# Optimization experiments

Hardware: AMD Instinct MI355X
Metric: run time of the kernel (lower is better)

Reference implementation:

```python
import jax, jax.numpy as jnp
import numpy as np
import math

A, B, C, D = 32, 32, 8, 16
K, STRIDE, PAD, ITERS = 3, 1, 1, 3
KK = K * K
KKA = KK * A


def squash(s, axis=-1):
    mag_sq = jnp.sum(s ** 2, axis=axis, keepdims=True)
    mag = jnp.sqrt(mag_sq)
    return mag_sq / (1.0 + mag_sq) * (s / mag)


def setup_inputs() -> dict:
    key = jax.random.key(0)
    k1, k2 = jax.random.split(key)
    pose = jax.random.normal(k1, (4, A * C, 14, 14), dtype=jnp.float32)
    # kaiming_uniform_ on (KKA, B*D, C): fan_in = (B*D)*C = 4096, bound = sqrt(6/fan_in)
    bound = math.sqrt(6.0 / (B * D * C))
    W = jax.random.uniform(k2, (KKA, B * D, C), dtype=jnp.float32, minval=-bound, maxval=bound)
    return {"pose": pose, "W": W}


def reference(pose, W):
    b, _, h, w = pose.shape
    # F.unfold equivalent: (b, A*C*kk, oh, ow), channel-major then kernel-position ordering
    patches = jax.lax.conv_general_dilated_patches(
        pose, (K, K), (STRIDE, STRIDE), [(PAD, PAD), (PAD, PAD)])
    l = patches.shape[2] * patches.shape[3]
    x = patches.reshape(b, A, C, KK, l)
    x = jnp.transpose(x, (0, 4, 3, 1, 2)).reshape(b, l, KKA, C)  # (b,l,kkA,C)
    # pose_out[b,l,k,:] = W[k] @ x[b,l,k]  -> (b,l,kkA,B*D)
    pose_out = jnp.einsum('kpc,blkc->blkp', W, x).reshape(b, l, KKA, B, D)
    logits = jnp.zeros((b, l, KKA, B, 1), dtype=pose.dtype)
    v = None
    for _ in range(ITERS):
        c = jax.nn.softmax(logits, axis=3)                      # over B capsules
        s = jnp.sum(c * pose_out, axis=2, keepdims=True)        # (b,l,1,B,D)
        v = squash(s)
        logits = logits + jnp.sum(v * pose_out, axis=-1, keepdims=True)
    v = v[:, :, 0]                                              # (b,l,B,D)
    v = jnp.transpose(v.reshape(b, l, B * D), (0, 2, 1))        # (b,B*D,l)
    oh = math.isqrt(l)
    return v.reshape(b, B * D, oh, oh)
```

## Files before the change

### kernel.cpp

```cpp
#include <hip/hip_runtime.h>
#include <stdint.h>

#define NSITES 784
#define LSZ    196
#define HWD    14
#define KKA_   288
#define BD_    512
#define NRG    6
#define ROWS_PER_BLK 48
#define NW     8
#define ROWS_PER_WAVE 6
#define SITES_PER_BLK 4
#define KC     6

#define WH_OFF    0
#define XH_OFF    2359296
#define WG_OFF    5971968
#define S1_OFF    8331264
#define PART_OFF  9936896
#define VBUF_OFF  19570688
#define WS_NEED   21176320

typedef _Float16 h2 __attribute__((ext_vector_type(2)));
typedef _Float16 h8 __attribute__((ext_vector_type(8)));
typedef float    f4 __attribute__((ext_vector_type(4)));

#define PIN8(p) asm volatile("" : "+v"(p[0]),"+v"(p[1]),"+v"(p[2]),"+v"(p[3]), \
                                  "+v"(p[4]),"+v"(p[5]),"+v"(p[6]),"+v"(p[7]))

__device__ __forceinline__ float dot8(const uint4 wv, const uint4 xv) {
    h2 w0 = __builtin_bit_cast(h2, wv.x), w1 = __builtin_bit_cast(h2, wv.y),
       w2 = __builtin_bit_cast(h2, wv.z), w3 = __builtin_bit_cast(h2, wv.w);
    h2 x0 = __builtin_bit_cast(h2, xv.x), x1 = __builtin_bit_cast(h2, xv.y),
       x2 = __builtin_bit_cast(h2, xv.z), x3 = __builtin_bit_cast(h2, xv.w);
#if __has_builtin(__builtin_amdgcn_fdot2)
    float acc = __builtin_amdgcn_fdot2(w0, x0, 0.f, false);
    acc = __builtin_amdgcn_fdot2(w1, x1, acc, false);
    acc = __builtin_amdgcn_fdot2(w2, x2, acc, false);
    acc = __builtin_amdgcn_fdot2(w3, x3, acc, false);
    return acc;
#else
    float acc = (float)w0.x*(float)x0.x + (float)w0.y*(float)x0.y
              + (float)w1.x*(float)x1.x + (float)w1.y*(float)x1.y
              + (float)w2.x*(float)x2.x + (float)w2.y*(float)x2.y
              + (float)w3.x*(float)x3.x + (float)w3.y*(float)x3.y;
    return acc;
#endif
}

__global__ __launch_bounds__(256) void k_prep(
    const float* __restrict__ pose, const float* __restrict__ W,
    uint4* __restrict__ Wh, uint4* __restrict__ xh, uint4* __restrict__ Wg)
{
    const int t  = threadIdx.x;
    const int bx = blockIdx.x;
    if (bx < NSITES) {
        const int site = bx;
        const int b = site / LSZ;
        const int l = site - b * LSZ;
        const int oh = l / HWD, ow = l - oh * HWD;
        for (int kk = t; kk < KKA_; kk += 256) {
            const int p = kk >> 5, a = kk & 31;
            const int ky = p / 3 - 1, kx = p % 3 - 1;
            const int y = oh + ky, x = ow + kx;
            const bool inb = (y >= 0 && y < HWD && x >= 0 && x < HWD);
            const float* pp = pose + ((size_t)b * 256 + a * 8) * LSZ
                            + (inb ? (y * HWD + x) : 0);
            uint32_t uo[4];
            #pragma unroll
            for (int cp = 0; cp < 4; ++cp) {
                const float f0 = inb ? pp[(2*cp)   * LSZ] : 0.f;
                const float f1 = inb ? pp[(2*cp+1) * LSZ] : 0.f;
                h2 hh; hh.x = (_Float16)f0; hh.y = (_Float16)f1;
                uo[cp] = __builtin_bit_cast(uint32_t, hh);
            }
            uint4 o; o.x = uo[0]; o.y = uo[1]; o.z = uo[2]; o.w = uo[3];
            xh[(size_t)site * KKA_ + kk] = o;
        }
    } else {
        const int wb = bx - NSITES;
        const int kk = wb * 4 + (t >> 6);
        const int ln = t & 63;
        const float* Wr = W + (size_t)kk * (BD_ * 8);
        #pragma unroll
        for (int u = 0; u < 8; ++u) {
            const int p = ln * 8 + u;
            const float4 fa = *(const float4*)(Wr + p * 8);
            const float4 fb = *(const float4*)(Wr + p * 8 + 4);
            uint32_t uo[4];
            h2 h0; h0.x=(_Float16)fa.x; h0.y=(_Float16)fa.y; uo[0]=__builtin_bit_cast(uint32_t,h0);
            h2 h1; h1.x=(_Float16)fa.z; h1.y=(_Float16)fa.w; uo[1]=__builtin_bit_cast(uint32_t,h1);
            h2 hv; hv.x=(_Float16)fb.x; hv.y=(_Float16)fb.y; uo[2]=__builtin_bit_cast(uint32_t,hv);
            h2 h3; h3.x=(_Float16)fb.z; h3.y=(_Float16)fb.w; uo[3]=__builtin_bit_cast(uint32_t,h3);
            uint4 o; o.x=uo[0]; o.y=uo[1]; o.z=uo[2]; o.w=uo[3];
            Wh[(size_t)kk * 512 + u * 64 + ln] = o;
            Wg[(size_t)kk * 512 + p] = o;
        }
    }
}

__global__ __launch_bounds__(256) void k_gemm1(
    const uint4* __restrict__ xh, const uint4* __restrict__ Wg,
    float* __restrict__ s1p)
{
    const int t   = threadIdx.x;
    const int w   = t >> 6;
    const int l   = t & 63;
    const int m0  = blockIdx.x * 16;
    const int n0  = blockIdx.y * 64 + w * 16;
    const int kc  = blockIdx.z;
    const int row = l & 15;
    const int sub = l >> 4;

    f4 acc = {0.f, 0.f, 0.f, 0.f};
    const uint4* ap = xh + (size_t)(m0 + row) * KKA_ + kc * 48 + sub;
    const uint4* bp = Wg + ((size_t)kc * 48 + sub) * 512 + (n0 + row);

    #pragma unroll
    for (int ks = 0; ks < 12; ++ks) {
        const h8 a = __builtin_bit_cast(h8, ap[ks * 4]);
        const h8 b = __builtin_bit_cast(h8, bp[(size_t)ks * 4 * 512]);
        acc = __builtin_amdgcn_mfma_f32_16x16x32_f16(a, b, acc, 0, 0, 0);
    }

    float* op = s1p + (size_t)kc * (NSITES * BD_)
              + (size_t)(m0 + sub * 4) * BD_ + n0 + row;
    op[0]        = acc[0];
    op[BD_]      = acc[1];
    op[2 * BD_]  = acc[2];
    op[3 * BD_]  = acc[3];
}

__global__ __launch_bounds__(256) void k_red1(
    const float* __restrict__ s1p, float* __restrict__ vbuf)
{
    const int site = blockIdx.x * 4 + (threadIdx.x >> 6);
    const int ln = threadIdx.x & 63;
    float tv[8] = {0.f,0.f,0.f,0.f,0.f,0.f,0.f,0.f};
    #pragma unroll
    for (int kc = 0; kc < KC; ++kc) {
        const float4* sp = (const float4*)(s1p + (size_t)kc * (NSITES * BD_)
                                           + (size_t)site * BD_ + ln * 8);
        const float4 a = sp[0], b = sp[1];
        tv[0]+=a.x; tv[1]+=a.y; tv[2]+=a.z; tv[3]+=a.w;
        tv[4]+=b.x; tv[5]+=b.y; tv[6]+=b.z; tv[7]+=b.w;
    }
    float msq = 0.f;
    #pragma unroll
    for (int j = 0; j < 8; ++j) { tv[j] *= (1.f / 32.f); msq += tv[j] * tv[j]; }
    msq += __shfl_xor(msq, 1, 64);
    const float fac = sqrtf(msq) / (1.f + msq);
    #pragma unroll
    for (int j = 0; j < 8; ++j) vbuf[(size_t)site * BD_ + ln * 8 + j] = tv[j] * fac;
}

template<int PASS>
__global__ __launch_bounds__(512, 4) void k_sweep(
    const uint4* __restrict__ Wh, const uint4* __restrict__ xh,
    const float* __restrict__ vbuf, float* __restrict__ partial)
{
    const int t  = threadIdx.x;
    const int w  = t >> 6;
    const int ln = t & 63;
    const int sg = blockIdx.x;
    const int rg = blockIdx.y;
    const int site0 = sg * SITES_PER_BLK;
    const int kk0 = __builtin_amdgcn_readfirstlane(rg * ROWS_PER_BLK + w);

    float v[SITES_PER_BLK][8];
    #pragma unroll
    for (int s = 0; s < SITES_PER_BLK; ++s) {
        const float4* vp = (const float4*)(vbuf + (size_t)(site0 + s) * BD_ + ln * 8);
        const float4 a = vp[0], bq = vp[1];
        v[s][0]=a.x;  v[s][1]=a.y;  v[s][2]=a.z;  v[s][3]=a.w;
        v[s][4]=bq.x; v[s][5]=bq.y; v[s][6]=bq.z; v[s][7]=bq.w;
        PIN8(v[s]);
    }

    float sacc[SITES_PER_BLK][8];
    #pragma unroll
    for (int s = 0; s < SITES_PER_BLK; ++s)
        #pragma unroll
        for (int j = 0; j < 8; ++j) sacc[s][j] = 0.f;

    const uint4* Wrow = Wh + (size_t)kk0 * 512;
    const uint4* xrow = xh + kk0;

    #pragma unroll 1
    for (int r = 0; r < ROWS_PER_WAVE; ++r) {
        uint4 wr[8];
        #pragma unroll
        for (int u = 0; u < 8; ++u) wr[u] = Wrow[u * 64 + ln];
        Wrow += NW * 512;

        #pragma unroll
        for (int s = 0; s < SITES_PER_BLK; ++s) {
            const uint4 xr = xrow[(size_t)(site0 + s) * KKA_];
            float po[8];
            #pragma unroll
            for (int j = 0; j < 8; ++j) po[j] = dot8(wr[j], xr);
            float up = v[s][0] * po[0];
            #pragma unroll
            for (int j = 1; j < 8; ++j) up += v[s][j] * po[j];
            up += __shfl_xor(up, 1, 64);
            const float e = __expf(up);
            float se = e;
            se += __shfl_xor(se, 2, 64);
            se += __shfl_xor(se, 4, 64);
            se += __shfl_xor(se, 8, 64);
            se += __shfl_xor(se, 16, 64);
            se += __shfl_xor(se, 32, 64);
            const float c = e * __builtin_amdgcn_rcpf(se);
            #pragma unroll
            for (int j = 0; j < 8; ++j) sacc[s][j] += c * po[j];
        }
        xrow += NW;
    }

    __shared__ float red[NW * BD_];
    #pragma unroll
    for (int s = 0; s < SITES_PER_BLK; ++s) {
        if (s) __syncthreads();
        float4 r0, r1;
        r0.x=sacc[s][0]; r0.y=sacc[s][1]; r0.z=sacc[s][2]; r0.w=sacc[s][3];
        r1.x=sacc[s][4]; r1.y=sacc[s][5]; r1.z=sacc[s][6]; r1.w=sacc[s][7];
        *(float4*)&red[w * BD_ + ln * 8]     = r0;
        *(float4*)&red[w * BD_ + ln * 8 + 4] = r1;
        __syncthreads();
        {
            const int p = t;
            float acc = red[p];
            #pragma unroll
            for (int ww = 1; ww < NW; ++ww) acc += red[ww * BD_ + p];
            partial[((size_t)(site0 + s) * NRG + rg) * BD_ + p] = acc;
        }
    }
}

template<int PASS>
__global__ __launch_bounds__(256) void k_reduce(
    const float* __restrict__ partial, float* __restrict__ vbuf,
    float* __restrict__ out)
{
    const int site = blockIdx.x * 4 + (threadIdx.x >> 6);
    const int ln = threadIdx.x & 63;
    float tv[8] = {0.f,0.f,0.f,0.f,0.f,0.f,0.f,0.f};
    #pragma unroll
    for (int rg = 0; rg < NRG; ++rg) {
        const float4* pp4 = (const float4*)(partial + ((size_t)site * NRG + rg) * BD_ + ln * 8);
        const float4 a = pp4[0], b = pp4[1];
        tv[0]+=a.x; tv[1]+=a.y; tv[2]+=a.z; tv[3]+=a.w;
        tv[4]+=b.x; tv[5]+=b.y; tv[6]+=b.z; tv[7]+=b.w;
    }
    float msq = 0.f;
    #pragma unroll
    for (int j = 0; j < 8; ++j) msq += tv[j] * tv[j];
    msq += __shfl_xor(msq, 1, 64);
    const float fac = sqrtf(msq) / (1.f + msq);
    if (PASS == 2) {
        #pragma unroll
        for (int j = 0; j < 8; ++j) vbuf[(size_t)site * BD_ + ln * 8 + j] += tv[j] * fac;
    } else {
        const int b = site / LSZ;
        const int l = site - b * LSZ;
        float* op = out + (size_t)b * BD_ * LSZ + l;
        #pragma unroll
        for (int j = 0; j < 8; ++j) op[(size_t)(ln * 8 + j) * LSZ] = tv[j] * fac;
    }
}

extern "C" void kernel_launch(void* const* d_in, const int* in_sizes, int n_in,
                              void* d_out, int out_size, void* d_ws, size_t ws_size,
                              hipStream_t stream) {
    const float* pose = (const float*)d_in[0];
    const float* W    = (const float*)d_in[1];
    float* out        = (float*)d_out;

    if (ws_size < (size_t)WS_NEED) return;

    uint8_t* ws = (uint8_t*)d_ws;
    uint4*  Wh     = (uint4*)  (ws + WH_OFF);
    uint4*  xh     = (uint4*)  (ws + XH_OFF);
    uint4*  Wg     = (uint4*)  (ws + WG_OFF);
    float* partial = (float*)  (ws + PART_OFF);
    float* vbuf    = (float*)  (ws + VBUF_OFF);

    k_prep<<<dim3(NSITES + 72), dim3(256), 0, stream>>>(pose, W, Wh, xh, Wg);

    k_gemm1<<<dim3(49, 8, KC), dim3(256), 0, stream>>>(xh, Wg, partial);
    k_red1<<<dim3(NSITES / 4), dim3(256), 0, stream>>>(partial, vbuf);

    const dim3 gs(NSITES / SITES_PER_BLK, NRG);
    k_sweep<2><<<gs, dim3(512), 0, stream>>>(Wh, xh, vbuf, partial);
    k_reduce<2><<<dim3(NSITES / 4), dim3(256), 0, stream>>>(partial, vbuf, out);
    k_sweep<3><<<gs, dim3(512), 0, stream>>>(Wh, xh, vbuf, partial);
    k_reduce<3><<<dim3(NSITES / 4), dim3(256), 0, stream>>>(partial, vbuf, out);
}
```

Baseline: 179.3 us.

## Repartition sweep into 8 row groups of 6 waves and linearize grids

The sweep kernel now uses 8 row groups of 36 rows with 6 waves (384 threads) per block instead of 6 groups of 48 rows with 8 waves, and the first GEMM splits K into 8 chunks instead of 6. Both grids are flattened to 1D, with the K-chunk or row-group index in the low bits so neighbouring blocks share the same sites/tiles for better L2 locality. The GEMM output moves to its own workspace buffer so it no longer aliases the partial buffer. This adds more blocks and more partials for the reduce kernels to sum, and the 512-wide cross-wave reduction now loops over 384 threads.

```diff
diff --git a/kernel.cpp b/kernel.cpp
--- a/kernel.cpp
+++ b/kernel.cpp
@@ -6,20 +6,20 @@
 #define HWD    14
 #define KKA_   288
 #define BD_    512
-#define NRG    6
-#define ROWS_PER_BLK 48
-#define NW     8
+#define NRG    8
+#define ROWS_PER_BLK 36
+#define NW     6
 #define ROWS_PER_WAVE 6
 #define SITES_PER_BLK 4
-#define KC     6
+#define KC     8
 
 #define WH_OFF    0
 #define XH_OFF    2359296
 #define WG_OFF    5971968
-#define S1_OFF    8331264
-#define PART_OFF  9936896
-#define VBUF_OFF  19570688
-#define WS_NEED   21176320
+#define GP_OFF    8331264
+#define PART_OFF  21176320
+#define VBUF_OFF  34021376
+#define WS_NEED   35627008
 
 typedef _Float16 h2 __attribute__((ext_vector_type(2)));
 typedef _Float16 h8 __attribute__((ext_vector_type(8)));
@@ -101,29 +101,33 @@
 
 __global__ __launch_bounds__(256) void k_gemm1(
     const uint4* __restrict__ xh, const uint4* __restrict__ Wg,
-    float* __restrict__ s1p)
-{
+    float* __restrict__ gp)
+{
+    const int bid = blockIdx.x;
+    const int kc  = bid & 7;
+    const int r2  = bid >> 3;
+    const int nb  = r2 & 7;
+    const int mb  = r2 >> 3;
     const int t   = threadIdx.x;
     const int w   = t >> 6;
     const int l   = t & 63;
-    const int m0  = blockIdx.x * 16;
-    const int n0  = blockIdx.y * 64 + w * 16;
-    const int kc  = blockIdx.z;
+    const int m0  = mb * 16;
+    const int n0  = nb * 64 + w * 16;
     const int row = l & 15;
     const int sub = l >> 4;
 
     f4 acc = {0.f, 0.f, 0.f, 0.f};
-    const uint4* ap = xh + (size_t)(m0 + row) * KKA_ + kc * 48 + sub;
-    const uint4* bp = Wg + ((size_t)kc * 48 + sub) * 512 + (n0 + row);
-
-    #pragma unroll
-    for (int ks = 0; ks < 12; ++ks) {
+    const uint4* ap = xh + (size_t)(m0 + row) * KKA_ + kc * 36 + sub;
+    const uint4* bp = Wg + ((size_t)kc * 36 + sub) * 512 + (n0 + row);
+
+    #pragma unroll
+    for (int ks = 0; ks < 9; ++ks) {
         const h8 a = __builtin_bit_cast(h8, ap[ks * 4]);
         const h8 b = __builtin_bit_cast(h8, bp[(size_t)ks * 4 * 512]);
         acc = __builtin_amdgcn_mfma_f32_16x16x32_f16(a, b, acc, 0, 0, 0);
     }
 
-    float* op = s1p + (size_t)kc * (NSITES * BD_)
+    float* op = gp + (size_t)kc * (NSITES * BD_)
               + (size_t)(m0 + sub * 4) * BD_ + n0 + row;
     op[0]        = acc[0];
     op[BD_]      = acc[1];
@@ -132,14 +136,14 @@
 }
 
 __global__ __launch_bounds__(256) void k_red1(
-    const float* __restrict__ s1p, float* __restrict__ vbuf)
+    const float* __restrict__ gp, float* __restrict__ vbuf)
 {
     const int site = blockIdx.x * 4 + (threadIdx.x >> 6);
     const int ln = threadIdx.x & 63;
     float tv[8] = {0.f,0.f,0.f,0.f,0.f,0.f,0.f,0.f};
     #pragma unroll
     for (int kc = 0; kc < KC; ++kc) {
-        const float4* sp = (const float4*)(s1p + (size_t)kc * (NSITES * BD_)
+        const float4* sp = (const float4*)(gp + (size_t)kc * (NSITES * BD_)
                                            + (size_t)site * BD_ + ln * 8);
         const float4 a = sp[0], b = sp[1];
         tv[0]+=a.x; tv[1]+=a.y; tv[2]+=a.z; tv[3]+=a.w;
@@ -155,15 +159,16 @@
 }
 
 template<int PASS>
-__global__ __launch_bounds__(512, 4) void k_sweep(
+__global__ __launch_bounds__(384, 4) void k_sweep(
     const uint4* __restrict__ Wh, const uint4* __restrict__ xh,
     const float* __restrict__ vbuf, float* __restrict__ partial)
 {
+    const int bid = blockIdx.x;
+    const int rg  = bid & 7;
+    const int sg  = bid >> 3;
     const int t  = threadIdx.x;
     const int w  = t >> 6;
     const int ln = t & 63;
-    const int sg = blockIdx.x;
-    const int rg = blockIdx.y;
     const int site0 = sg * SITES_PER_BLK;
     const int kk0 = __builtin_amdgcn_readfirstlane(rg * ROWS_PER_BLK + w);
 
@@ -227,8 +232,7 @@
         *(float4*)&red[w * BD_ + ln * 8]     = r0;
         *(float4*)&red[w * BD_ + ln * 8 + 4] = r1;
         __syncthreads();
-        {
-            const int p = t;
+        for (int p = t; p < BD_; p += 384) {
             float acc = red[p];
             #pragma unroll
             for (int ww = 1; ww < NW; ++ww) acc += red[ww * BD_ + p];
@@ -282,17 +286,18 @@
     uint4*  Wh     = (uint4*)  (ws + WH_OFF);
     uint4*  xh     = (uint4*)  (ws + XH_OFF);
     uint4*  Wg     = (uint4*)  (ws + WG_OFF);
+    float*  gp     = (float*)  (ws + GP_OFF);
     float* partial = (float*)  (ws + PART_OFF);
     float* vbuf    = (float*)  (ws + VBUF_OFF);
 
     k_prep<<<dim3(NSITES + 72), dim3(256), 0, stream>>>(pose, W, Wh, xh, Wg);
 
-    k_gemm1<<<dim3(49, 8, KC), dim3(256), 0, stream>>>(xh, Wg, partial);
-    k_red1<<<dim3(NSITES / 4), dim3(256), 0, stream>>>(partial, vbuf);
-
-    const dim3 gs(NSITES / SITES_PER_BLK, NRG);
-    k_sweep<2><<<gs, dim3(512), 0, stream>>>(Wh, xh, vbuf, partial);
+    k_gemm1<<<dim3(49 * 8 * KC), dim3(256), 0, stream>>>(xh, Wg, gp);
+    k_red1<<<dim3(NSITES / 4), dim3(256), 0, stream>>>(gp, vbuf);
+
+    const dim3 gs(196 * NRG);
+    k_sweep<2><<<gs, dim3(384), 0, stream>>>(Wh, xh, vbuf, partial);
     k_reduce<2><<<dim3(NSITES / 4), dim3(256), 0, stream>>>(partial, vbuf, out);
-    k_sweep<3><<<gs, dim3(512), 0, stream>>>(Wh, xh, vbuf, partial);
+    k_sweep<3><<<gs, dim3(384), 0, stream>>>(Wh, xh, vbuf, partial);
     k_reduce<3><<<dim3(NSITES / 4), dim3(256), 0, stream>>>(partial, vbuf, out);
 }
```

New measurement: 203.9 us. 13.7% more time.

## Coalesce pose unfold reads in prep and stage x tiles in LDS for gemm1

Applied to the files above, without the earlier changes.

The prep kernel's unfold is remapped so each block handles one (batch, kernel-position, capsule) triple and its threads walk the 196 spatial sites. Consecutive threads now read adjacent pose addresses instead of strided ones, but the xh writes become strided. The gemm1 kernel first loads its 16x48 x tile into padded LDS, so the four waves share one global load instead of each fetching it. This costs a block barrier and some LDS. An unused offset define is dropped and a parameter renamed.

```diff
diff --git a/kernel.cpp b/kernel.cpp
--- a/kernel.cpp
+++ b/kernel.cpp
@@ -16,7 +16,6 @@
 #define WH_OFF    0
 #define XH_OFF    2359296
 #define WG_OFF    5971968
-#define S1_OFF    8331264
 #define PART_OFF  9936896
 #define VBUF_OFF  19570688
 #define WS_NEED   21176320
@@ -54,14 +53,14 @@
 {
     const int t  = threadIdx.x;
     const int bx = blockIdx.x;
-    if (bx < NSITES) {
-        const int site = bx;
-        const int b = site / LSZ;
-        const int l = site - b * LSZ;
-        const int oh = l / HWD, ow = l - oh * HWD;
-        for (int kk = t; kk < KKA_; kk += 256) {
-            const int p = kk >> 5, a = kk & 31;
-            const int ky = p / 3 - 1, kx = p % 3 - 1;
+    if (bx < 4 * KKA_) {
+        const int b  = bx / KKA_;
+        const int kk = bx - b * KKA_;
+        const int p  = kk >> 5, a = kk & 31;
+        const int ky = p / 3 - 1, kx = p % 3 - 1;
+        if (t < LSZ) {
+            const int l  = t;
+            const int oh = l / HWD, ow = l - oh * HWD;
             const int y = oh + ky, x = ow + kx;
             const bool inb = (y >= 0 && y < HWD && x >= 0 && x < HWD);
             const float* pp = pose + ((size_t)b * 256 + a * 8) * LSZ
@@ -75,10 +74,10 @@
                 uo[cp] = __builtin_bit_cast(uint32_t, hh);
             }
             uint4 o; o.x = uo[0]; o.y = uo[1]; o.z = uo[2]; o.w = uo[3];
-            xh[(size_t)site * KKA_ + kk] = o;
+            xh[((size_t)b * LSZ + l) * KKA_ + kk] = o;
         }
     } else {
-        const int wb = bx - NSITES;
+        const int wb = bx - 4 * KKA_;
         const int kk = wb * 4 + (t >> 6);
         const int ln = t & 63;
         const float* Wr = W + (size_t)kk * (BD_ * 8);
@@ -101,7 +100,7 @@
 
 __global__ __launch_bounds__(256) void k_gemm1(
     const uint4* __restrict__ xh, const uint4* __restrict__ Wg,
-    float* __restrict__ s1p)
+    float* __restrict__ gp)
 {
     const int t   = threadIdx.x;
     const int w   = t >> 6;
@@ -112,18 +111,26 @@
     const int row = l & 15;
     const int sub = l >> 4;
 
+    __shared__ uint4 x_lds[16][49];
+    #pragma unroll
+    for (int q = 0; q < 3; ++q) {
+        const int idx = t + 256 * q;
+        const int r = idx / 48, i = idx - r * 48;
+        x_lds[r][i] = xh[(size_t)(m0 + r) * KKA_ + kc * 48 + i];
+    }
+    __syncthreads();
+
     f4 acc = {0.f, 0.f, 0.f, 0.f};
-    const uint4* ap = xh + (size_t)(m0 + row) * KKA_ + kc * 48 + sub;
     const uint4* bp = Wg + ((size_t)kc * 48 + sub) * 512 + (n0 + row);
 
     #pragma unroll
     for (int ks = 0; ks < 12; ++ks) {
-        const h8 a = __builtin_bit_cast(h8, ap[ks * 4]);
+        const h8 a = __builtin_bit_cast(h8, x_lds[row][sub + ks * 4]);
         const h8 b = __builtin_bit_cast(h8, bp[(size_t)ks * 4 * 512]);
         acc = __builtin_amdgcn_mfma_f32_16x16x32_f16(a, b, acc, 0, 0, 0);
     }
 
-    float* op = s1p + (size_t)kc * (NSITES * BD_)
+    float* op = gp + (size_t)kc * (NSITES * BD_)
               + (size_t)(m0 + sub * 4) * BD_ + n0 + row;
     op[0]        = acc[0];
     op[BD_]      = acc[1];
@@ -132,14 +139,14 @@
 }
 
 __global__ __launch_bounds__(256) void k_red1(
-    const float* __restrict__ s1p, float* __restrict__ vbuf)
+    const float* __restrict__ gp, float* __restrict__ vbuf)
 {
     const int site = blockIdx.x * 4 + (threadIdx.x >> 6);
     const int ln = threadIdx.x & 63;
     float tv[8] = {0.f,0.f,0.f,0.f,0.f,0.f,0.f,0.f};
     #pragma unroll
     for (int kc = 0; kc < KC; ++kc) {
-        const float4* sp = (const float4*)(s1p + (size_t)kc * (NSITES * BD_)
+        const float4* sp = (const float4*)(gp + (size_t)kc * (NSITES * BD_)
                                            + (size_t)site * BD_ + ln * 8);
         const float4 a = sp[0], b = sp[1];
         tv[0]+=a.x; tv[1]+=a.y; tv[2]+=a.z; tv[3]+=a.w;
@@ -285,7 +292,7 @@
     float* partial = (float*)  (ws + PART_OFF);
     float* vbuf    = (float*)  (ws + VBUF_OFF);
 
-    k_prep<<<dim3(NSITES + 72), dim3(256), 0, stream>>>(pose, W, Wh, xh, Wg);
+    k_prep<<<dim3(4 * KKA_ + 72), dim3(256), 0, stream>>>(pose, W, Wh, xh, Wg);
 
     k_gemm1<<<dim3(49, 8, KC), dim3(256), 0, stream>>>(xh, Wg, partial);
     k_red1<<<dim3(NSITES / 4), dim3(256), 0, stream>>>(partial, vbuf);
```

New measurement: 170.6 us. 1.05x faster.
